# Kernel optimization log

Hardware: AMD Instinct MI355X
Metric: run time of the kernel (lower is better)

The kernel has to match this reference:

```python
import jax, jax.numpy as jnp
import numpy as np

EPS = 1e-12  # torch F.normalize eps

def l2norm(x, axis=-1):
    n = jnp.linalg.norm(x, axis=axis, keepdims=True)
    return x / jnp.maximum(n, EPS)

def setup_inputs() -> dict:
    key = jax.random.key(0)
    ks = jax.random.split(key, 8)
    n_vocab, d, n_asp = 100000, 256, 14
    B, L, M = 512, 100, 10
    pos = jax.random.randint(ks[0], (B, L), 0, n_vocab)
    negs = jax.random.randint(ks[1], (B, M, L), 0, n_vocab)
    E_w = jax.random.normal(ks[2], (n_vocab, d), dtype=jnp.float32) * 0.1
    T_w = jax.random.normal(ks[3], (n_asp, d), dtype=jnp.float32) * 0.1
    M_w = jax.random.uniform(ks[4], (d, d), dtype=jnp.float32, minval=-0.1, maxval=0.1)
    M_b = jnp.zeros((d,), dtype=jnp.float32)
    lin_w = jax.random.normal(ks[5], (n_asp, d), dtype=jnp.float32) * 0.05
    lin_b = jnp.zeros((n_asp,), dtype=jnp.float32)
    return {"pos": pos, "negs": negs, "E_w": E_w, "T_w": T_w,
            "M_w": M_w, "M_b": M_b, "lin_w": lin_w, "lin_b": lin_b}

def reference(pos, negs, E_w, T_w, M_w, M_b, lin_w, lin_b):
    # e: [B, L, d] (original keeps e_i as [B, d, L]; layout differs, math identical)
    e = E_w[pos]
    y_s = jnp.mean(e, axis=1)                    # mean over tokens -> [B, d]
    My = y_s @ M_w.T + M_b                       # [B, d]
    d_i = jnp.tanh(jnp.einsum('bld,bd->bl', e, My))  # [B, L]
    # NOTE: original normalizes exp(d_i) by the GLOBAL sum over the whole batch
    a_i = jnp.exp(d_i) / jnp.sum(jnp.exp(d_i))   # [B, L]
    z_s = l2norm(jnp.einsum('bld,bl->bd', e, a_i))   # [B, d]
    p_t = jax.nn.softmax(z_s @ lin_w.T + lin_b, axis=1)  # [B, n_asp]
    r_s = l2norm(p_t @ T_w)                      # [B, d]
    e_n = E_w[negs]                              # [B, M, L, d]
    z_n = l2norm(jnp.mean(e_n, axis=2))          # [B, M, d]
    return (r_s, z_s, z_n)
```

## Files before the change

kernel.cpp:

```cpp
#include <hip/hip_runtime.h>
#include <math.h>

#define D 256

__device__ __forceinline__ float wave_reduce_sum(float v) {
#pragma unroll
    for (int off = 32; off > 0; off >>= 1) v += __shfl_xor(v, off);
    return v;
}
__device__ __forceinline__ float wave_reduce_max(float v) {
#pragma unroll
    for (int off = 32; off > 0; off >>= 1) v = fmaxf(v, __shfl_xor(v, off));
    return v;
}

__device__ __forceinline__ float4 load_row_f32(const float* __restrict__ E_w,
                                               int idx, int lane) {
    return ((const float4*)(E_w + (size_t)idx * D))[lane];
}
__device__ __forceinline__ float4 load_row_i8(const signed char* __restrict__ Eq,
                                              const float* __restrict__ scales,
                                              int idx, int lane) {
    const char4 c = ((const char4*)(Eq + (size_t)idx * D))[lane];
    const float f = scales[idx];
    return make_float4(f * (float)c.x, f * (float)c.y,
                       f * (float)c.z, f * (float)c.w);
}
template <bool I8>
__device__ __forceinline__ float4 load_row(const float* __restrict__ E_w,
                                           const signed char* __restrict__ Eq,
                                           const float* __restrict__ scales,
                                           int idx, int lane) {
    return I8 ? load_row_i8(Eq, scales, idx, lane) : load_row_f32(E_w, idx, lane);
}

__global__ __launch_bounds__(256) void convert_i8_kernel(
    const float* __restrict__ E_w, signed char* __restrict__ Eq,
    float* __restrict__ scales, int n_vocab) {
    const int lane = threadIdx.x & 63;
    const int gw   = (blockIdx.x * 256 + threadIdx.x) >> 6;
    const int nw   = (gridDim.x * 256) >> 6;

    for (int r0 = gw * 4; r0 < n_vocab; r0 += nw * 4) {
        const int n = min(4, n_vocab - r0);
        float4 v[4];
#pragma unroll
        for (int k = 0; k < 4; ++k)
            if (k < n) v[k] = load_row_f32(E_w, r0 + k, lane);
#pragma unroll
        for (int k = 0; k < 4; ++k) {
            if (k >= n) break;
            float mx = fmaxf(fmaxf(fabsf(v[k].x), fabsf(v[k].y)),
                             fmaxf(fabsf(v[k].z), fabsf(v[k].w)));
            mx = wave_reduce_max(mx);
            const float inv = (mx > 0.f) ? 127.f / mx : 0.f;
            int qx = __float2int_rn(v[k].x * inv);
            int qy = __float2int_rn(v[k].y * inv);
            int qz = __float2int_rn(v[k].z * inv);
            int qw = __float2int_rn(v[k].w * inv);
            const unsigned int packed =
                ((unsigned int)(unsigned char)(signed char)qx) |
                ((unsigned int)(unsigned char)(signed char)qy << 8) |
                ((unsigned int)(unsigned char)(signed char)qz << 16) |
                ((unsigned int)(unsigned char)(signed char)qw << 24);
            ((unsigned int*)(Eq + (size_t)(r0 + k) * D))[lane] = packed;
            if (lane == 0) scales[r0 + k] = mx * (1.f / 127.f);
        }
    }
}

template <bool I8>
__global__ __launch_bounds__(256) void abae_fused_kernel(
    const int* __restrict__ pos, const int* __restrict__ negs,
    const float* __restrict__ E_w, const signed char* __restrict__ Eq,
    const float* __restrict__ scales, const float* __restrict__ T_w,
    const float* __restrict__ M_w, const float* __restrict__ M_b,
    const float* __restrict__ lin_w, const float* __restrict__ lin_b,
    float* __restrict__ r_s, float* __restrict__ z_s, float* __restrict__ z_n,
    int B, int L, int n_asp) {
    const int t    = threadIdx.x;
    const int lane = t & 63;
    const int wv   = t >> 6;

    __shared__ float4 sred[4][64];
    __shared__ float  sy[D];
    __shared__ float  smy[D];
    __shared__ float  slog[16];
    __shared__ float  sp[16];
    __shared__ float  sscal[4];

    const int C = (L + 3) / 4;

    if (blockIdx.x >= B) {
        const int bm = blockIdx.x - B;
        const int* __restrict__ idxp = negs + (size_t)bm * L;
        const int s0 = wv * C;
        const int e0 = min(L, s0 + C);

        float4 acc = make_float4(0.f, 0.f, 0.f, 0.f);
        int l = s0;
        for (; l + 5 <= e0; l += 5) {
            const int i0 = idxp[l], i1 = idxp[l + 1], i2 = idxp[l + 2],
                      i3 = idxp[l + 3], i4 = idxp[l + 4];
            const float4 v0 = load_row<I8>(E_w, Eq, scales, i0, lane);
            const float4 v1 = load_row<I8>(E_w, Eq, scales, i1, lane);
            const float4 v2 = load_row<I8>(E_w, Eq, scales, i2, lane);
            const float4 v3 = load_row<I8>(E_w, Eq, scales, i3, lane);
            const float4 v4 = load_row<I8>(E_w, Eq, scales, i4, lane);
            acc.x += v0.x + v1.x + v2.x + v3.x + v4.x;
            acc.y += v0.y + v1.y + v2.y + v3.y + v4.y;
            acc.z += v0.z + v1.z + v2.z + v3.z + v4.z;
            acc.w += v0.w + v1.w + v2.w + v3.w + v4.w;
        }
        for (; l < e0; ++l) {
            const float4 v = load_row<I8>(E_w, Eq, scales, idxp[l], lane);
            acc.x += v.x; acc.y += v.y; acc.z += v.z; acc.w += v.w;
        }
        sred[wv][lane] = acc;
        __syncthreads();
        if (wv == 0) {
            float4 z  = sred[0][lane];
            const float4 a1 = sred[1][lane], a2 = sred[2][lane], a3 = sred[3][lane];
            const float invL = 1.f / (float)L;
            z.x = (z.x + a1.x + a2.x + a3.x) * invL;
            z.y = (z.y + a1.y + a2.y + a3.y) * invL;
            z.z = (z.z + a1.z + a2.z + a3.z) * invL;
            z.w = (z.w + a1.w + a2.w + a3.w) * invL;
            float ss = z.x * z.x + z.y * z.y + z.z * z.z + z.w * z.w;
            ss = wave_reduce_sum(ss);
            const float inv = 1.f / fmaxf(sqrtf(ss), 1e-12f);
            z.x *= inv; z.y *= inv; z.z *= inv; z.w *= inv;
            ((float4*)(z_n + (size_t)bm * D))[lane] = z;
        }
        return;
    }

    const int b = blockIdx.x;
    const int* __restrict__ posb = pos + (size_t)b * L;
    const int s0 = wv * C;
    const int e0 = min(L, s0 + C);

    float4 acc = make_float4(0.f, 0.f, 0.f, 0.f);
    int l = s0;
    for (; l + 4 <= e0; l += 4) {
        const int i0 = posb[l], i1 = posb[l + 1], i2 = posb[l + 2], i3 = posb[l + 3];
        const float4 v0 = load_row<I8>(E_w, Eq, scales, i0, lane);
        const float4 v1 = load_row<I8>(E_w, Eq, scales, i1, lane);
        const float4 v2 = load_row<I8>(E_w, Eq, scales, i2, lane);
        const float4 v3 = load_row<I8>(E_w, Eq, scales, i3, lane);
        acc.x += v0.x + v1.x + v2.x + v3.x;
        acc.y += v0.y + v1.y + v2.y + v3.y;
        acc.z += v0.z + v1.z + v2.z + v3.z;
        acc.w += v0.w + v1.w + v2.w + v3.w;
    }
    for (; l < e0; ++l) {
        const float4 v = load_row<I8>(E_w, Eq, scales, posb[l], lane);
        acc.x += v.x; acc.y += v.y; acc.z += v.z; acc.w += v.w;
    }
    sred[wv][lane] = acc;
    __syncthreads();
    if (wv == 0) {
        float4 y  = sred[0][lane];
        const float4 a1 = sred[1][lane], a2 = sred[2][lane], a3 = sred[3][lane];
        const float invL = 1.f / (float)L;
        y.x = (y.x + a1.x + a2.x + a3.x) * invL;
        y.y = (y.y + a1.y + a2.y + a3.y) * invL;
        y.z = (y.z + a1.z + a2.z + a3.z) * invL;
        y.w = (y.w + a1.w + a2.w + a3.w) * invL;
        ((float4*)sy)[lane] = y;
    }
    __syncthreads();

    {
        const float4 y4 = ((const float4*)sy)[lane];
        for (int r0 = wv * 64; r0 < wv * 64 + 64; r0 += 4) {
            const float4 m0 = ((const float4*)(M_w + (size_t)(r0 + 0) * D))[lane];
            const float4 m1 = ((const float4*)(M_w + (size_t)(r0 + 1) * D))[lane];
            const float4 m2 = ((const float4*)(M_w + (size_t)(r0 + 2) * D))[lane];
            const float4 m3 = ((const float4*)(M_w + (size_t)(r0 + 3) * D))[lane];
            float p0 = m0.x * y4.x + m0.y * y4.y + m0.z * y4.z + m0.w * y4.w;
            float p1 = m1.x * y4.x + m1.y * y4.y + m1.z * y4.z + m1.w * y4.w;
            float p2 = m2.x * y4.x + m2.y * y4.y + m2.z * y4.z + m2.w * y4.w;
            float p3 = m3.x * y4.x + m3.y * y4.y + m3.z * y4.z + m3.w * y4.w;
#pragma unroll
            for (int off = 32; off > 0; off >>= 1) {
                p0 += __shfl_xor(p0, off);
                p1 += __shfl_xor(p1, off);
                p2 += __shfl_xor(p2, off);
                p3 += __shfl_xor(p3, off);
            }
            if (lane == 0) {
                smy[r0 + 0] = p0 + M_b[r0 + 0];
                smy[r0 + 1] = p1 + M_b[r0 + 1];
                smy[r0 + 2] = p2 + M_b[r0 + 2];
                smy[r0 + 3] = p3 + M_b[r0 + 3];
            }
        }
    }
    __syncthreads();

    const float4 my4 = ((const float4*)smy)[lane];
    float4 zacc = make_float4(0.f, 0.f, 0.f, 0.f);
    l = s0;
    for (; l + 1 < e0; l += 2) {
        const float4 ea = load_row<I8>(E_w, Eq, scales, posb[l], lane);
        const float4 eb = load_row<I8>(E_w, Eq, scales, posb[l + 1], lane);
        float pa = ea.x * my4.x + ea.y * my4.y + ea.z * my4.z + ea.w * my4.w;
        float pb = eb.x * my4.x + eb.y * my4.y + eb.z * my4.z + eb.w * my4.w;
#pragma unroll
        for (int off = 32; off > 0; off >>= 1) {
            pa += __shfl_xor(pa, off);
            pb += __shfl_xor(pb, off);
        }
        const float wa = expf(tanhf(pa));
        const float wb = expf(tanhf(pb));
        zacc.x += ea.x * wa + eb.x * wb;
        zacc.y += ea.y * wa + eb.y * wb;
        zacc.z += ea.z * wa + eb.z * wb;
        zacc.w += ea.w * wa + eb.w * wb;
    }
    for (; l < e0; ++l) {
        const float4 ea = load_row<I8>(E_w, Eq, scales, posb[l], lane);
        float pa = ea.x * my4.x + ea.y * my4.y + ea.z * my4.z + ea.w * my4.w;
        pa = wave_reduce_sum(pa);
        const float wa = expf(tanhf(pa));
        zacc.x += ea.x * wa; zacc.y += ea.y * wa;
        zacc.z += ea.z * wa; zacc.w += ea.w * wa;
    }
    sred[wv][lane] = zacc;
    __syncthreads();
    if (wv == 0) {
        float4 z  = sred[0][lane];
        const float4 a1 = sred[1][lane], a2 = sred[2][lane], a3 = sred[3][lane];
        z.x += a1.x + a2.x + a3.x;
        z.y += a1.y + a2.y + a3.y;
        z.z += a1.z + a2.z + a3.z;
        z.w += a1.w + a2.w + a3.w;
        float ss = z.x * z.x + z.y * z.y + z.z * z.z + z.w * z.w;
        ss = wave_reduce_sum(ss);
        const float inv = 1.f / fmaxf(sqrtf(ss), 1e-12f);
        z.x *= inv; z.y *= inv; z.z *= inv; z.w *= inv;
        ((float4*)(z_s + (size_t)b * D))[lane] = z;
        ((float4*)sy)[lane] = z;
    }
    __syncthreads();

    const float4 z4 = ((const float4*)sy)[lane];
    for (int a = wv; a < n_asp; a += 4) {
        const float4 w4 = ((const float4*)(lin_w + (size_t)a * D))[lane];
        float p = z4.x * w4.x + z4.y * w4.y + z4.z * w4.z + z4.w * w4.w;
        p = wave_reduce_sum(p);
        if (lane == 0) slog[a] = p + lin_b[a];
    }
    __syncthreads();
    if (t == 0) {
        float mx = -1e30f;
        for (int a = 0; a < n_asp; ++a) mx = fmaxf(mx, slog[a]);
        float s = 0.f;
        for (int a = 0; a < n_asp; ++a) {
            const float e = expf(slog[a] - mx);
            sp[a] = e; s += e;
        }
        const float invs = 1.f / s;
        for (int a = 0; a < n_asp; ++a) sp[a] *= invs;
    }
    __syncthreads();

    float r = 0.f;
    for (int a = 0; a < n_asp; ++a) r += sp[a] * T_w[(size_t)a * D + t];
    const float sq = wave_reduce_sum(r * r);
    if (lane == 0) sscal[wv] = sq;
    __syncthreads();
    const float tot = sscal[0] + sscal[1] + sscal[2] + sscal[3];
    const float inv = 1.f / fmaxf(sqrtf(tot), 1e-12f);
    r_s[(size_t)b * D + t] = r * inv;
}

extern "C" void kernel_launch(void* const* d_in, const int* in_sizes, int n_in,
                              void* d_out, int out_size, void* d_ws, size_t ws_size,
                              hipStream_t stream) {
    const int*   pos   = (const int*)d_in[0];
    const int*   negs  = (const int*)d_in[1];
    const float* E_w   = (const float*)d_in[2];
    const float* T_w   = (const float*)d_in[3];
    const float* M_w   = (const float*)d_in[4];
    const float* M_b   = (const float*)d_in[5];
    const float* lin_w = (const float*)d_in[6];
    const float* lin_b = (const float*)d_in[7];
    float* out = (float*)d_out;

    const int d       = in_sizes[5];
    const int n_asp   = in_sizes[7];
    const int M       = in_sizes[1] / in_sizes[0];
    const int B       = out_size / (d * (2 + M));
    const int L       = in_sizes[0] / B;
    const int n_vocab = in_sizes[2] / d;
    (void)n_in;

    float* r_s = out;
    float* z_s = out + (size_t)B * d;
    float* z_n = out + (size_t)2 * B * d;

    const size_t need = (size_t)n_vocab * D + (size_t)n_vocab * sizeof(float);
    const bool use_i8 = ws_size >= need;

    signed char* Eq = (signed char*)d_ws;
    float* scales   = (float*)(Eq + (size_t)n_vocab * D);

    if (use_i8) {
        convert_i8_kernel<<<2048, 256, 0, stream>>>(E_w, Eq, scales, n_vocab);
        abae_fused_kernel<true><<<B + B * M, 256, 0, stream>>>(
            pos, negs, E_w, Eq, scales, T_w, M_w, M_b, lin_w, lin_b,
            r_s, z_s, z_n, B, L, n_asp);
    } else {
        abae_fused_kernel<false><<<B + B * M, 256, 0, stream>>>(
            pos, negs, E_w, (const signed char*)nullptr, (const float*)nullptr,
            T_w, M_w, M_b, lin_w, lin_b, r_s, z_s, z_n, B, L, n_asp);
    }
}
```

Measured before the change: 217.0 us.

## Assign one wave per negative sample and schedule negative blocks first

Negative-sample blocks now give each wave its own (b,m) row and have it sum all L tokens with 10-wide unrolled gathers. This removes the shared-memory cross-wave reduction and the __syncthreads from that path, and cuts the block count by four. Negative blocks are moved to the front of the grid, ahead of the positive blocks. The positive path unrolls by 5 instead of 4. Each wave now runs a longer serial loop, which could lower latency hiding per wave.

```diff
diff --git a/kernel.cpp b/kernel.cpp
--- a/kernel.cpp
+++ b/kernel.cpp
@@ -54,10 +54,10 @@
                              fmaxf(fabsf(v[k].z), fabsf(v[k].w)));
             mx = wave_reduce_max(mx);
             const float inv = (mx > 0.f) ? 127.f / mx : 0.f;
-            int qx = __float2int_rn(v[k].x * inv);
-            int qy = __float2int_rn(v[k].y * inv);
-            int qz = __float2int_rn(v[k].z * inv);
-            int qw = __float2int_rn(v[k].w * inv);
+            const int qx = __float2int_rn(v[k].x * inv);
+            const int qy = __float2int_rn(v[k].y * inv);
+            const int qz = __float2int_rn(v[k].z * inv);
+            const int qw = __float2int_rn(v[k].w * inv);
             const unsigned int packed =
                 ((unsigned int)(unsigned char)(signed char)qx) |
                 ((unsigned int)(unsigned char)(signed char)qy << 8) |
@@ -77,7 +77,7 @@
     const float* __restrict__ M_w, const float* __restrict__ M_b,
     const float* __restrict__ lin_w, const float* __restrict__ lin_b,
     float* __restrict__ r_s, float* __restrict__ z_s, float* __restrict__ z_n,
-    int B, int L, int n_asp) {
+    int B, int BM, int nbneg, int L, int n_asp) {
     const int t    = threadIdx.x;
     const int lane = t & 63;
     const int wv   = t >> 6;
@@ -89,69 +89,61 @@
     __shared__ float  sp[16];
     __shared__ float  sscal[4];
 
-    const int C = (L + 3) / 4;
-
-    if (blockIdx.x >= B) {
-        const int bm = blockIdx.x - B;
-        const int* __restrict__ idxp = negs + (size_t)bm * L;
-        const int s0 = wv * C;
-        const int e0 = min(L, s0 + C);
-
-        float4 acc = make_float4(0.f, 0.f, 0.f, 0.f);
-        int l = s0;
-        for (; l + 5 <= e0; l += 5) {
-            const int i0 = idxp[l], i1 = idxp[l + 1], i2 = idxp[l + 2],
-                      i3 = idxp[l + 3], i4 = idxp[l + 4];
-            const float4 v0 = load_row<I8>(E_w, Eq, scales, i0, lane);
-            const float4 v1 = load_row<I8>(E_w, Eq, scales, i1, lane);
-            const float4 v2 = load_row<I8>(E_w, Eq, scales, i2, lane);
-            const float4 v3 = load_row<I8>(E_w, Eq, scales, i3, lane);
-            const float4 v4 = load_row<I8>(E_w, Eq, scales, i4, lane);
-            acc.x += v0.x + v1.x + v2.x + v3.x + v4.x;
-            acc.y += v0.y + v1.y + v2.y + v3.y + v4.y;
-            acc.z += v0.z + v1.z + v2.z + v3.z + v4.z;
-            acc.w += v0.w + v1.w + v2.w + v3.w + v4.w;
-        }
-        for (; l < e0; ++l) {
-            const float4 v = load_row<I8>(E_w, Eq, scales, idxp[l], lane);
-            acc.x += v.x; acc.y += v.y; acc.z += v.z; acc.w += v.w;
-        }
-        sred[wv][lane] = acc;
-        __syncthreads();
-        if (wv == 0) {
-            float4 z  = sred[0][lane];
-            const float4 a1 = sred[1][lane], a2 = sred[2][lane], a3 = sred[3][lane];
+    if (blockIdx.x < (unsigned)nbneg) {
+        const int bm = blockIdx.x * 4 + wv;
+        if (bm < BM) {
+            const int* __restrict__ idxp = negs + (size_t)bm * L;
+            float4 acc = make_float4(0.f, 0.f, 0.f, 0.f);
+            int l = 0;
+            for (; l + 10 <= L; l += 10) {
+                int id[10];
+#pragma unroll
+                for (int k = 0; k < 10; ++k) id[k] = idxp[l + k];
+                float4 v[10];
+#pragma unroll
+                for (int k = 0; k < 10; ++k)
+                    v[k] = load_row<I8>(E_w, Eq, scales, id[k], lane);
+#pragma unroll
+                for (int k = 0; k < 10; ++k) {
+                    acc.x += v[k].x; acc.y += v[k].y;
+                    acc.z += v[k].z; acc.w += v[k].w;
+                }
+            }
+            for (; l < L; ++l) {
+                const float4 v = load_row<I8>(E_w, Eq, scales, idxp[l], lane);
+                acc.x += v.x; acc.y += v.y; acc.z += v.z; acc.w += v.w;
+            }
             const float invL = 1.f / (float)L;
-            z.x = (z.x + a1.x + a2.x + a3.x) * invL;
-            z.y = (z.y + a1.y + a2.y + a3.y) * invL;
-            z.z = (z.z + a1.z + a2.z + a3.z) * invL;
-            z.w = (z.w + a1.w + a2.w + a3.w) * invL;
-            float ss = z.x * z.x + z.y * z.y + z.z * z.z + z.w * z.w;
+            acc.x *= invL; acc.y *= invL; acc.z *= invL; acc.w *= invL;
+            float ss = acc.x * acc.x + acc.y * acc.y + acc.z * acc.z + acc.w * acc.w;
             ss = wave_reduce_sum(ss);
             const float inv = 1.f / fmaxf(sqrtf(ss), 1e-12f);
-            z.x *= inv; z.y *= inv; z.z *= inv; z.w *= inv;
-            ((float4*)(z_n + (size_t)bm * D))[lane] = z;
+            acc.x *= inv; acc.y *= inv; acc.z *= inv; acc.w *= inv;
+            ((float4*)(z_n + (size_t)bm * D))[lane] = acc;
         }
         return;
     }
 
-    const int b = blockIdx.x;
+    const int b = blockIdx.x - nbneg;
     const int* __restrict__ posb = pos + (size_t)b * L;
+    const int C  = (L + 3) / 4;
     const int s0 = wv * C;
     const int e0 = min(L, s0 + C);
 
     float4 acc = make_float4(0.f, 0.f, 0.f, 0.f);
     int l = s0;
-    for (; l + 4 <= e0; l += 4) {
-        const int i0 = posb[l], i1 = posb[l + 1], i2 = posb[l + 2], i3 = posb[l + 3];
+    for (; l + 5 <= e0; l += 5) {
+        const int i0 = posb[l], i1 = posb[l + 1], i2 = posb[l + 2],
+                  i3 = posb[l + 3], i4 = posb[l + 4];
         const float4 v0 = load_row<I8>(E_w, Eq, scales, i0, lane);
         const float4 v1 = load_row<I8>(E_w, Eq, scales, i1, lane);
         const float4 v2 = load_row<I8>(E_w, Eq, scales, i2, lane);
         const float4 v3 = load_row<I8>(E_w, Eq, scales, i3, lane);
-        acc.x += v0.x + v1.x + v2.x + v3.x;
-        acc.y += v0.y + v1.y + v2.y + v3.y;
-        acc.z += v0.z + v1.z + v2.z + v3.z;
-        acc.w += v0.w + v1.w + v2.w + v3.w;
+        const float4 v4 = load_row<I8>(E_w, Eq, scales, i4, lane);
+        acc.x += v0.x + v1.x + v2.x + v3.x + v4.x;
+        acc.y += v0.y + v1.y + v2.y + v3.y + v4.y;
+        acc.z += v0.z + v1.z + v2.z + v3.z + v4.z;
+        acc.w += v0.w + v1.w + v2.w + v3.w + v4.w;
     }
     for (; l < e0; ++l) {
         const float4 v = load_row<I8>(E_w, Eq, scales, posb[l], lane);
@@ -301,6 +293,9 @@
     float* z_s = out + (size_t)B * d;
     float* z_n = out + (size_t)2 * B * d;
 
+    const int BM    = B * M;
+    const int nbneg = (BM + 3) / 4;
+
     const size_t need = (size_t)n_vocab * D + (size_t)n_vocab * sizeof(float);
     const bool use_i8 = ws_size >= need;
 
@@ -309,12 +304,12 @@
 
     if (use_i8) {
         convert_i8_kernel<<<2048, 256, 0, stream>>>(E_w, Eq, scales, n_vocab);
-        abae_fused_kernel<true><<<B + B * M, 256, 0, stream>>>(
+        abae_fused_kernel<true><<<nbneg + B, 256, 0, stream>>>(
             pos, negs, E_w, Eq, scales, T_w, M_w, M_b, lin_w, lin_b,
-            r_s, z_s, z_n, B, L, n_asp);
+            r_s, z_s, z_n, B, BM, nbneg, L, n_asp);
     } else {
-        abae_fused_kernel<false><<<B + B * M, 256, 0, stream>>>(
+        abae_fused_kernel<false><<<nbneg + B, 256, 0, stream>>>(
             pos, negs, E_w, (const signed char*)nullptr, (const float*)nullptr,
-            T_w, M_w, M_b, lin_w, lin_b, r_s, z_s, z_n, B, L, n_asp);
-    }
-}
+            T_w, M_w, M_b, lin_w, lin_b, r_s, z_s, z_n, B, BM, nbneg, L, n_asp);
+    }
+}
```

New measurement: 228.5 us. +5.3%, slower.
